# Optimization experiments

Hardware: AMD Instinct MI355X
Metric: run time of the kernel (lower is better)

The kernel has to match this reference:

```python
import jax, jax.numpy as jnp
import numpy as np

N = 131072   # tokens per expert slot
E = 8        # local_experts
D = 128      # expert feature dim (Linear(D, D) expert)


def setup_inputs() -> dict:
    key = jax.random.key(0)
    k1, k2, k3 = jax.random.split(key, 3)
    inputs = jax.random.normal(k1, (N, E, D), dtype=jnp.float32)
    # per-expert Linear(D, D) parameters, stacked along the expert axis
    scale = 1.0 / np.sqrt(D)
    W = jax.random.uniform(k2, (E, D, D), dtype=jnp.float32, minval=-scale, maxval=scale)
    b = jax.random.uniform(k3, (E, D), dtype=jnp.float32, minval=-scale, maxval=scale)
    return {"inputs": inputs, "W": W, "b": b}


def reference(inputs, W, b):
    # SeqExperts.forward with expert_input_nums=None:
    #   split inputs [N, E, D] into E chunks [N, 1, D] along dim=1,
    #   apply expert_e (Linear) to chunk e, concat on dim=1.
    # Expressed as one batched einsum over the expert axis (same math).
    out = jnp.einsum('ned,edf->nef', inputs, W) + b[None, :, :]
    return out
```

## Files before the change

kernel.cpp:

```cpp
#include <hip/hip_runtime.h>

#define NTOK 131072
#define NEXP 8
#define NDIM 128

typedef __bf16 bf16x8 __attribute__((ext_vector_type(8)));
typedef float f32x4 __attribute__((ext_vector_type(4)));
typedef unsigned short u16x8 __attribute__((ext_vector_type(8)));

union PackAB { u16x8 u; bf16x8 b; };

__device__ __forceinline__ unsigned short f2bf(float f) {
    unsigned int u = __float_as_uint(f);
    u += 0x7FFFu + ((u >> 16) & 1u);
    return (unsigned short)(u >> 16);
}

__global__ __launch_bounds__(256) void seq_experts_kernel(
    const float* __restrict__ inp,
    const float* __restrict__ W,
    const float* __restrict__ bias,
    float* __restrict__ out)
{
    __shared__ unsigned short Wt[NDIM * NDIM];

    const int e    = blockIdx.y;
    const int tid  = threadIdx.x;
    const int wave = tid >> 6;
    const int lane = tid & 63;
    const int quad = lane >> 4;
    const int l16  = lane & 15;

    {
        const float* We = W + (size_t)e * (NDIM * NDIM);
        const int f    = tid & 127;
        const int half = tid >> 7;
        #pragma unroll
        for (int kb = 0; kb < 8; ++kb) {
            const int KB = half * 8 + kb;
            PackAB pk;
            #pragma unroll
            for (int j = 0; j < 8; ++j)
                pk.u[j] = f2bf(We[(size_t)(KB * 8 + j) * NDIM + f]);
            *(u16x8*)&Wt[f * NDIM + ((KB ^ (f & 15)) << 3)] = pk.u;
        }
    }

    const int rowbase = blockIdx.x * 128 + wave * 32;
    bf16x8 afrag[2][4];
    #pragma unroll
    for (int rt = 0; rt < 2; ++rt) {
        const int n = rowbase + rt * 16 + l16;
        const float* arow = inp + ((size_t)n * NEXP + e) * NDIM;
        #pragma unroll
        for (int ks = 0; ks < 4; ++ks) {
            const float* p = arow + ks * 32 + quad * 8;
            float4 x = *(const float4*)(p);
            float4 y = *(const float4*)(p + 4);
            PackAB pk;
            pk.u[0] = f2bf(x.x); pk.u[1] = f2bf(x.y);
            pk.u[2] = f2bf(x.z); pk.u[3] = f2bf(x.w);
            pk.u[4] = f2bf(y.x); pk.u[5] = f2bf(y.y);
            pk.u[6] = f2bf(y.z); pk.u[7] = f2bf(y.w);
            afrag[rt][ks] = pk.b;
        }
    }

    __syncthreads();

    f32x4 acc[2][8] = {};
    #pragma unroll
    for (int ks = 0; ks < 4; ++ks) {
        const int kb = ks * 4 + quad;
        #pragma unroll
        for (int ct = 0; ct < 8; ++ct) {
            const int f = ct * 16 + l16;
            PackAB pk;
            pk.u = *(const u16x8*)&Wt[f * NDIM + ((kb ^ l16) << 3)];
            const bf16x8 bfrag = pk.b;
            acc[0][ct] = __builtin_amdgcn_mfma_f32_16x16x32_bf16(afrag[0][ks], bfrag, acc[0][ct], 0, 0, 0);
            acc[1][ct] = __builtin_amdgcn_mfma_f32_16x16x32_bf16(afrag[1][ks], bfrag, acc[1][ct], 0, 0, 0);
        }
    }

    const float* be = bias + e * NDIM;
    #pragma unroll
    for (int ct = 0; ct < 8; ++ct) {
        const float bv = be[ct * 16 + l16];
        #pragma unroll
        for (int rt = 0; rt < 2; ++rt) {
            const int n0 = rowbase + rt * 16 + quad * 4;
            float* po = out + ((size_t)n0 * NEXP + e) * NDIM + ct * 16 + l16;
            #pragma unroll
            for (int r = 0; r < 4; ++r)
                po[(size_t)r * (NEXP * NDIM)] = acc[rt][ct][r] + bv;
        }
    }
}

extern "C" void kernel_launch(void* const* d_in, const int* in_sizes, int n_in,
                              void* d_out, int out_size, void* d_ws, size_t ws_size,
                              hipStream_t stream) {
    const float* inp  = (const float*)d_in[0];
    const float* W    = (const float*)d_in[1];
    const float* bb   = (const float*)d_in[2];
    float* out = (float*)d_out;
    dim3 grid(NTOK / 128, NEXP);
    seq_experts_kernel<<<grid, dim3(256), 0, stream>>>(inp, W, bb, out);
}
```

Before: 978.2 us.

## Loop persistent token tiles per block, swap MFMA operands for vector stores

```diff
diff --git a/kernel.cpp b/kernel.cpp
--- a/kernel.cpp
+++ b/kernel.cpp
@@ -3,6 +3,8 @@
 #define NTOK 131072
 #define NEXP 8
 #define NDIM 128
+#define TPB  8
+#define TOKS_PER_TILE 64
 
 typedef __bf16 bf16x8 __attribute__((ext_vector_type(8)));
 typedef float f32x4 __attribute__((ext_vector_type(4)));
@@ -10,13 +12,7 @@
 
 union PackAB { u16x8 u; bf16x8 b; };
 
-__device__ __forceinline__ unsigned short f2bf(float f) {
-    unsigned int u = __float_as_uint(f);
-    u += 0x7FFFu + ((u >> 16) & 1u);
-    return (unsigned short)(u >> 16);
-}
-
-__global__ __launch_bounds__(256) void seq_experts_kernel(
+__global__ __launch_bounds__(256, 5) void seq_experts_kernel(
     const float* __restrict__ inp,
     const float* __restrict__ W,
     const float* __restrict__ bias,
@@ -41,60 +37,54 @@
             PackAB pk;
             #pragma unroll
             for (int j = 0; j < 8; ++j)
-                pk.u[j] = f2bf(We[(size_t)(KB * 8 + j) * NDIM + f]);
+                pk.b[j] = (__bf16)We[(size_t)(KB * 8 + j) * NDIM + f];
             *(u16x8*)&Wt[f * NDIM + ((KB ^ (f & 15)) << 3)] = pk.u;
         }
     }
+    __syncthreads();
 
-    const int rowbase = blockIdx.x * 128 + wave * 32;
-    bf16x8 afrag[2][4];
-    #pragma unroll
-    for (int rt = 0; rt < 2; ++rt) {
-        const int n = rowbase + rt * 16 + l16;
-        const float* arow = inp + ((size_t)n * NEXP + e) * NDIM;
+    const float*  be         = bias + e * NDIM;
+    const size_t  row_stride = (size_t)NEXP * NDIM;
+
+    for (int t = 0; t < TPB; ++t) {
+        const int n = (blockIdx.x * TPB + t) * TOKS_PER_TILE + wave * 16 + l16;
+        const float* arow = inp + (size_t)n * row_stride + e * NDIM + quad * 8;
+
+        bf16x8 afrag[4];
         #pragma unroll
         for (int ks = 0; ks < 4; ++ks) {
-            const float* p = arow + ks * 32 + quad * 8;
-            float4 x = *(const float4*)(p);
-            float4 y = *(const float4*)(p + 4);
+            float4 x = *(const float4*)(arow + ks * 32);
+            float4 y = *(const float4*)(arow + ks * 32 + 4);
             PackAB pk;
-            pk.u[0] = f2bf(x.x); pk.u[1] = f2bf(x.y);
-            pk.u[2] = f2bf(x.z); pk.u[3] = f2bf(x.w);
-            pk.u[4] = f2bf(y.x); pk.u[5] = f2bf(y.y);
-            pk.u[6] = f2bf(y.z); pk.u[7] = f2bf(y.w);
-            afrag[rt][ks] = pk.b;
+            pk.b[0] = (__bf16)x.x; pk.b[1] = (__bf16)x.y;
+            pk.b[2] = (__bf16)x.z; pk.b[3] = (__bf16)x.w;
+            pk.b[4] = (__bf16)y.x; pk.b[5] = (__bf16)y.y;
+            pk.b[6] = (__bf16)y.z; pk.b[7] = (__bf16)y.w;
+            afrag[ks] = pk.b;
         }
-    }
 
-    __syncthreads();
+        f32x4 acc[8];
+        #pragma unroll
+        for (int ct = 0; ct < 8; ++ct)
+            acc[ct] = *(const f32x4*)(be + ct * 16 + quad * 4);
 
-    f32x4 acc[2][8] = {};
-    #pragma unroll
-    for (int ks = 0; ks < 4; ++ks) {
-        const int kb = ks * 4 + quad;
         #pragma unroll
-        for (int ct = 0; ct < 8; ++ct) {
-            const int f = ct * 16 + l16;
-            PackAB pk;
-            pk.u = *(const u16x8*)&Wt[f * NDIM + ((kb ^ l16) << 3)];
-            const bf16x8 bfrag = pk.b;
-            acc[0][ct] = __builtin_amdgcn_mfma_f32_16x16x32_bf16(afrag[0][ks], bfrag, acc[0][ct], 0, 0, 0);
-            acc[1][ct] = __builtin_amdgcn_mfma_f32_16x16x32_bf16(afrag[1][ks], bfrag, acc[1][ct], 0, 0, 0);
+        for (int ks = 0; ks < 4; ++ks) {
+            const int kb = ks * 4 + quad;
+            #pragma unroll
+            for (int ct = 0; ct < 8; ++ct) {
+                const int f = ct * 16 + l16;
+                PackAB pk;
+                pk.u = *(const u16x8*)&Wt[f * NDIM + ((kb ^ l16) << 3)];
+                acc[ct] = __builtin_amdgcn_mfma_f32_16x16x32_bf16(
+                              pk.b, afrag[ks], acc[ct], 0, 0, 0);
+            }
         }
-    }
 
-    const float* be = bias + e * NDIM;
-    #pragma unroll
-    for (int ct = 0; ct < 8; ++ct) {
-        const float bv = be[ct * 16 + l16];
+        float* orow = out + (size_t)n * row_stride + e * NDIM + quad * 4;
         #pragma unroll
-        for (int rt = 0; rt < 2; ++rt) {
-            const int n0 = rowbase + rt * 16 + quad * 4;
-            float* po = out + ((size_t)n0 * NEXP + e) * NDIM + ct * 16 + l16;
-            #pragma unroll
-            for (int r = 0; r < 4; ++r)
-                po[(size_t)r * (NEXP * NDIM)] = acc[rt][ct][r] + bv;
-        }
+        for (int ct = 0; ct < 8; ++ct)
+            *(f32x4*)(orow + ct * 16) = acc[ct];
     }
 }
 
@@ -105,6 +95,6 @@
     const float* W    = (const float*)d_in[1];
     const float* bb   = (const float*)d_in[2];
     float* out = (float*)d_out;
-    dim3 grid(NTOK / 128, NEXP);
+    dim3 grid(NTOK / (TPB * TOKS_PER_TILE), NEXP);
     seq_experts_kernel<<<grid, dim3(256), 0, stream>>>(inp, W, bb, out);
 }
```

Measured after the change: 1.243 ms. 1.27x slower.
